# Performance work log

Hardware: AMD Instinct MI355X
Metric: run time of the kernel (lower is better)

## Reference

```python
import jax, jax.numpy as jnp
import numpy as np

DIM = 192
HEADS = 6
HEAD_DIM = 32
WS = 7          # window_size
DISP = WS // 2  # cyclic-shift displacement = 3
NEG = -1e9      # large negative instead of -inf (grad-safe, numerically equivalent)


def _rel_indices():
    idx = np.array([[x, y] for x in range(WS) for y in range(WS)])  # [WS^2, 2]
    d = idx[None, :, :] - idx[:, None, :] + WS - 1                  # [WS^2, WS^2, 2]
    return d


def _shift_masks():
    n = WS * WS
    ul = np.zeros((n, n), dtype=np.float32)
    ul[-DISP * WS:, :-DISP * WS] = NEG
    ul[:-DISP * WS, -DISP * WS:] = NEG
    lr = np.zeros((WS, WS, WS, WS), dtype=np.float32)
    lr[:, -DISP:, :, :-DISP] = NEG
    lr[:, :-DISP, :, -DISP:] = NEG
    lr = lr.reshape(n, n)
    return ul, lr


def setup_inputs() -> dict:
    key = jax.random.key(0)
    k1, k2, k3, k4, k5 = jax.random.split(key, 5)
    inner = HEADS * HEAD_DIM
    B, H, W = 32, 56, 56
    x = jax.random.normal(k1, (B, H, W, DIM), dtype=jnp.float32)
    w_qkv = jax.random.normal(k2, (DIM, inner * 3), dtype=jnp.float32) * (DIM ** -0.5)
    w_out = jax.random.normal(k3, (inner, DIM), dtype=jnp.float32) * (inner ** -0.5)
    b_out = jnp.zeros((DIM,), dtype=jnp.float32)
    pos_emb = jax.random.normal(k4, (2 * WS - 1, 2 * WS - 1), dtype=jnp.float32)
    return {"x": x, "w_qkv": w_qkv, "w_out": w_out, "b_out": b_out, "pos_emb": pos_emb}


def _forward(x, w_qkv, w_out, b_out, pos_emb):
    b, n_h, n_w, _ = x.shape
    nw_h, nw_w = n_h // WS, n_w // WS
    nw = nw_h * nw_w
    n = WS * WS
    scale = HEAD_DIM ** -0.5

    # cyclic shift
    x = jnp.roll(x, shift=(-DISP, -DISP), axis=(1, 2))

    qkv = x @ w_qkv  # [b, H, W, 3*inner]
    qkv = qkv.reshape(b, nw_h, WS, nw_w, WS, 3, HEADS, HEAD_DIM)
    # -> [3, b, heads, nw, WS*WS, head_dim]
    qkv = qkv.transpose(5, 0, 6, 1, 3, 2, 4, 7).reshape(3, b, HEADS, nw, n, HEAD_DIM)
    q, k, v = qkv[0], qkv[1], qkv[2]

    dots = jnp.einsum('bhwid,bhwjd->bhwij', q, k) * scale  # [b,h,nw,n,n]

    rel = _rel_indices()
    bias = pos_emb[rel[:, :, 0], rel[:, :, 1]]  # [n, n]
    dots = dots + bias

    # shifted-window masks: last row of windows gets UL mask, last column gets LR mask
    ul, lr = _shift_masks()
    madd = jnp.zeros((nw, n, n), dtype=dots.dtype)
    madd = madd.at[-nw_w:].add(jnp.asarray(ul))
    madd = madd.at[nw_w - 1::nw_w].add(jnp.asarray(lr))
    dots = dots + madd

    attn = jax.nn.softmax(dots, axis=-1)
    out = jnp.einsum('bhwij,bhwjd->bhwid', attn, v)  # [b,h,nw,n,hd]

    # un-window: -> [b, H, W, inner]
    out = out.reshape(b, HEADS, nw_h, nw_w, WS, WS, HEAD_DIM)
    out = out.transpose(0, 2, 4, 3, 5, 1, 6).reshape(b, n_h, n_w, HEADS * HEAD_DIM)
    out = out @ w_out + b_out

    # cyclic back-shift
    out = jnp.roll(out, shift=(DISP, DISP), axis=(1, 2))
    return out


def reference(x, w_qkv, w_out, b_out, pos_emb):
    return _forward(x, w_qkv, w_out, b_out, pos_emb)
```

## Files before the change

kernel.cpp:

```cpp
#include <hip/hip_runtime.h>
#include <hip/hip_bf16.h>


typedef __bf16 bf16x8 __attribute__((ext_vector_type(8)));
typedef __bf16 bf16x4 __attribute__((ext_vector_type(4)));
typedef float f32x4 __attribute__((ext_vector_type(4)));
using bf = __bf16;

#define MFMA16(a, b, c) __builtin_amdgcn_mfma_f32_16x16x32_bf16((a), (b), (c), 0, 0, 0)

static constexpr float kNEG = -1000000000.0f;
static constexpr float kScale = 0.17677669529663687f;

static constexpr size_t OFF_WQKVT = 0;
static constexpr size_t OFF_WOUTT = 221184;
static constexpr size_t OFF_TBL   = 294912;

static constexpr int QK_STRIDE = 40;
static constexpr int VT_STRIDE = 72;
static constexpr int X_STRIDE  = 200;
static constexpr int O_STRIDE  = 200;
static constexpr int P_STRIDE  = 72;
static constexpr int TB_STRIDE = 68;
static constexpr int R0_OFF = 0;
static constexpr int R1_OFF = 23552;
static constexpr int R2_OFF = 47104;
static constexpr int TB_OFF = 74752;
static constexpr int LDS_BYTES = TB_OFF + 49 * TB_STRIDE * 2 + 8;

__device__ __forceinline__ unsigned pack2(float a, float b) {
  union { bf h[2]; unsigned u; } cv;
  cv.h[0] = (bf)a; cv.h[1] = (bf)b;
  return cv.u;
}

__global__ void prep_kernel(const float* __restrict__ wqkv, const float* __restrict__ wout,
                            const float* __restrict__ pos, char* __restrict__ ws) {
  bf* wqkvT = (bf*)(ws + OFF_WQKVT);
  bf* woutT = (bf*)(ws + OFF_WOUTT);
  float* tbl = (float*)(ws + OFF_TBL);
  int tid = blockIdx.x * blockDim.x + threadIdx.x;
  int nthr = gridDim.x * blockDim.x;
  for (int i = tid; i < 192 * 576; i += nthr) {
    int k = i / 576, n = i % 576;
    wqkvT[n * 192 + k] = (bf)wqkv[i];
  }
  for (int i = tid; i < 192 * 192; i += nthr) {
    int k = i / 192, n = i % 192;
    woutT[n * 192 + k] = (bf)wout[i];
  }
  for (int i = tid; i < 4 * 64 * 64; i += nthr) {
    int type = i >> 12, rem = i & 4095, r = rem >> 6, c = rem & 63;
    float v;
    if (r < 49 && c < 49) {
      int ix = r / 7, iy = r % 7, jx = c / 7, jy = c % 7;
      v = pos[(jx - ix + 6) * 13 + (jy - iy + 6)];
      if ((type & 1) && ((r >= 28) != (c >= 28))) v += kNEG;
      if ((type & 2) && ((iy >= 4) != (jy >= 4))) v += kNEG;
    } else {
      v = kNEG;
    }
    tbl[i] = v;
  }
}

__global__ __launch_bounds__(512, 4) void fused_kernel(const float* __restrict__ x,
                                                       const float* __restrict__ bout,
                                                       const char* __restrict__ ws,
                                                       float* __restrict__ out) {
  __shared__ __align__(16) char smem[LDS_BYTES];
  bf* Xl = (bf*)(smem + R0_OFF);
  bf* Ql = (bf*)(smem + R0_OFF);
  bf* Pl = (bf*)(smem + R0_OFF);
  bf* Kl = (bf*)(smem + R1_OFF);
  bf* Ol = (bf*)(smem + R1_OFF);
  bf* Vl = (bf*)(smem + R2_OFF);
  bf* Tb = (bf*)(smem + TB_OFF);

  const bf* wqkvT = (const bf*)(ws + OFF_WQKVT);
  const bf* woutT = (const bf*)(ws + OFF_WOUTT);

  int bw = blockIdx.x;
  int b = bw >> 6, win = bw & 63;
  int wh = win >> 3, wwi = win & 7;
  int type = ((wh == 7) ? 1 : 0) | ((wwi == 7) ? 2 : 0);
  const float* tblg = (const float*)(ws + OFF_TBL) + type * 4096;

  int tid = threadIdx.x;
  int wave = tid >> 6, lane = tid & 63;
  int l15 = lane & 15, g = lane >> 4;
  int mrow = wave >> 2, ncol = wave & 3;

#pragma unroll
  for (int it = 0; it < 3; ++it) {
    int chunk = it * 512 + tid;
    if (chunk < 1176) {
      int r = chunk / 24, c8 = (chunk % 24) * 8;
      int tr = r / 7, tc = r % 7;
      int h = wh * 7 + tr + 3; if (h >= 56) h -= 56;
      int w = wwi * 7 + tc + 3; if (w >= 56) w -= 56;
      const float* p = x + (((size_t)b * 56 + h) * 56 + w) * 192 + c8;
      bf16x8 v;
#pragma unroll
      for (int j = 0; j < 8; ++j) v[j] = (bf)p[j];
      *(bf16x8*)(Xl + r * X_STRIDE + c8) = v;
    }
  }
  if (tid < 392) {
    int r = tid >> 3, c8 = (tid & 7) * 8;
    const float* p = tblg + r * 64 + c8;
    bf16x4 v0, v1;
#pragma unroll
    for (int j = 0; j < 4; ++j) { v0[j] = (bf)p[j]; v1[j] = (bf)p[4 + j]; }
    *(bf16x4*)(Tb + r * TB_STRIDE + c8) = v0;
    *(bf16x4*)(Tb + r * TB_STRIDE + c8 + 4) = v1;
  }
  __syncthreads();

  {
    f32x4 acc[2][6] = {};
#pragma unroll
    for (int ks = 0; ks < 6; ++ks) {
      bf16x8 a[2];
#pragma unroll
      for (int mt = 0; mt < 2; ++mt) {
        int t = mrow * 32 + mt * 16 + l15; if (t > 48) t = 48;
        a[mt] = *(const bf16x8*)(Xl + t * X_STRIDE + ks * 32 + g * 8);
      }
#pragma unroll
      for (int nt = 0; nt < 6; ++nt) {
        int n = 192 + ncol * 96 + nt * 16 + l15;
        bf16x8 bfr = *(const bf16x8*)(wqkvT + (size_t)n * 192 + ks * 32 + g * 8);
#pragma unroll
        for (int mt = 0; mt < 2; ++mt) acc[mt][nt] = MFMA16(a[mt], bfr, acc[mt][nt]);
      }
    }
#pragma unroll
    for (int nt = 0; nt < 6; ++nt) {
      int n = 192 + ncol * 96 + nt * 16 + l15;
      int s3 = n / 192;
      int lc = n - s3 * 192;
      int hd = lc >> 5, d = lc & 31;
#pragma unroll
      for (int mt = 0; mt < 2; ++mt) {
#pragma unroll
        for (int r = 0; r < 4; ++r) {
          int t = mrow * 32 + mt * 16 + 4 * g + r;
          bf bv = (bf)acc[mt][nt][r];
          if (s3 == 1) { if (t < 49) Kl[(hd * 49 + t) * QK_STRIDE + d] = bv; }
          else         { Vl[(hd * 32 + d) * VT_STRIDE + t] = bv; }
        }
      }
    }
  }

  {
    f32x4 qacc[2][3] = {};
#pragma unroll
    for (int ks = 0; ks < 6; ++ks) {
      bf16x8 a[2];
#pragma unroll
      for (int mt = 0; mt < 2; ++mt) {
        int t = mrow * 32 + mt * 16 + l15; if (t > 48) t = 48;
        a[mt] = *(const bf16x8*)(Xl + t * X_STRIDE + ks * 32 + g * 8);
      }
#pragma unroll
      for (int nt = 0; nt < 3; ++nt) {
        int n = ncol * 48 + nt * 16 + l15;
        bf16x8 bfr = *(const bf16x8*)(wqkvT + (size_t)n * 192 + ks * 32 + g * 8);
#pragma unroll
        for (int mt = 0; mt < 2; ++mt) qacc[mt][nt] = MFMA16(a[mt], bfr, qacc[mt][nt]);
      }
    }
    __syncthreads();
#pragma unroll
    for (int nt = 0; nt < 3; ++nt) {
      int n = ncol * 48 + nt * 16 + l15;
      int hd = n >> 5, d = n & 31;
#pragma unroll
      for (int mt = 0; mt < 2; ++mt) {
#pragma unroll
        for (int r = 0; r < 4; ++r) {
          int t = mrow * 32 + mt * 16 + 4 * g + r;
          if (t < 49) Ql[(hd * 49 + t) * QK_STRIDE + d] = (bf)qacc[mt][nt][r];
        }
      }
    }
  }
  __syncthreads();

  unsigned pp[3][8];
#pragma unroll
  for (int ii = 0; ii < 3; ++ii) {
    int item = wave + ii * 8;
    int head = item >> 2, mq = item & 3;
    const bf* Qh = Ql + head * 49 * QK_STRIDE;
    const bf* Kh = Kl + head * 49 * QK_STRIDE;

    int tq = mq * 16 + l15; if (tq > 48) tq = 48;
    bf16x8 qf = *(const bf16x8*)(Qh + tq * QK_STRIDE + g * 8);
    f32x4 sa[4];
#pragma unroll
    for (int nt = 0; nt < 4; ++nt) {
      int tk = nt * 16 + l15; if (tk > 48) tk = 48;
      bf16x8 kf = *(const bf16x8*)(Kh + tk * QK_STRIDE + g * 8);
      f32x4 z = {};
      sa[nt] = MFMA16(qf, kf, z);
    }
#pragma unroll
    for (int r = 0; r < 4; ++r) {
      int rowc = mq * 16 + 4 * g + r; if (rowc > 48) rowc = 48;
      const bf* trow = Tb + rowc * TB_STRIDE + l15;
#pragma unroll
      for (int nt = 0; nt < 4; ++nt)
        sa[nt][r] = sa[nt][r] * kScale + (float)trow[nt * 16];
    }

#pragma unroll
    for (int r = 0; r < 4; ++r) {
      float m = fmaxf(fmaxf(sa[0][r], sa[1][r]), fmaxf(sa[2][r], sa[3][r]));
#pragma unroll
      for (int off = 1; off < 16; off <<= 1) m = fmaxf(m, __shfl_xor(m, off));
      float p0 = __expf(sa[0][r] - m), p1 = __expf(sa[1][r] - m);
      float p2 = __expf(sa[2][r] - m), p3 = __expf(sa[3][r] - m);
      float sum = p0 + p1 + p2 + p3;
#pragma unroll
      for (int off = 1; off < 16; off <<= 1) sum += __shfl_xor(sum, off);
      float rinv = 1.0f / sum;
      pp[ii][r * 2]     = pack2(p0 * rinv, p1 * rinv);
      pp[ii][r * 2 + 1] = pack2(p2 * rinv, p3 * rinv);
    }
  }
  __syncthreads();

  bf* Pw = Pl + wave * 16 * P_STRIDE;
  for (int ii = 0; ii < 3; ++ii) {
    int item = wave + ii * 8;
    int head = item >> 2, mq = item & 3;
    const bf* Vh = Vl + head * 32 * VT_STRIDE;

#pragma unroll
    for (int r = 0; r < 4; ++r) {
      int prow = 4 * g + r;
      union { unsigned u; bf h[2]; } ua, ub;
      ua.u = pp[ii][r * 2]; ub.u = pp[ii][r * 2 + 1];
      Pw[prow * P_STRIDE + l15]      = ua.h[0];
      Pw[prow * P_STRIDE + 16 + l15] = ua.h[1];
      Pw[prow * P_STRIDE + 32 + l15] = ub.h[0];
      Pw[prow * P_STRIDE + 48 + l15] = ub.h[1];
    }
    asm volatile("s_waitcnt lgkmcnt(0)" ::: "memory");
    __builtin_amdgcn_sched_barrier(0);

    f32x4 o0 = {}, o1 = {};
#pragma unroll
    for (int ks = 0; ks < 2; ++ks) {
      bf16x8 pf = *(const bf16x8*)(Pw + l15 * P_STRIDE + ks * 32 + g * 8);
      bf16x8 v0 = *(const bf16x8*)(Vh + l15 * VT_STRIDE + ks * 32 + g * 8);
      bf16x8 v1 = *(const bf16x8*)(Vh + (16 + l15) * VT_STRIDE + ks * 32 + g * 8);
      o0 = MFMA16(pf, v0, o0);
      o1 = MFMA16(pf, v1, o1);
    }
#pragma unroll
    for (int r = 0; r < 4; ++r) {
      int orow = mq * 16 + 4 * g + r;
      if (orow < 49) {
        Ol[orow * O_STRIDE + head * 32 + l15]      = (bf)o0[r];
        Ol[orow * O_STRIDE + head * 32 + 16 + l15] = (bf)o1[r];
      }
    }
    asm volatile("s_waitcnt lgkmcnt(0)" ::: "memory");
    __builtin_amdgcn_sched_barrier(0);
  }
  __syncthreads();

  f32x4 pacc[2][3] = {};
#pragma unroll
  for (int ks = 0; ks < 6; ++ks) {
    int t0 = mrow * 32 + l15;      if (t0 > 48) t0 = 48;
    int t1 = mrow * 32 + 16 + l15; if (t1 > 48) t1 = 48;
    bf16x8 a0 = *(const bf16x8*)(Ol + t0 * O_STRIDE + ks * 32 + g * 8);
    bf16x8 a1 = *(const bf16x8*)(Ol + t1 * O_STRIDE + ks * 32 + g * 8);
#pragma unroll
    for (int nt = 0; nt < 3; ++nt) {
      bf16x8 bfr = *(const bf16x8*)(woutT + (size_t)(ncol * 48 + nt * 16 + l15) * 192 + ks * 32 + g * 8);
      pacc[0][nt] = MFMA16(a0, bfr, pacc[0][nt]);
      pacc[1][nt] = MFMA16(a1, bfr, pacc[1][nt]);
    }
  }
#pragma unroll
  for (int nt = 0; nt < 3; ++nt) {
    int col = ncol * 48 + nt * 16 + l15;
    float bo = bout[col];
#pragma unroll
    for (int mt = 0; mt < 2; ++mt) {
#pragma unroll
      for (int r = 0; r < 4; ++r) {
        int t = mrow * 32 + mt * 16 + 4 * g + r;
        if (t < 49) {
          int tr = t / 7, tc = t % 7;
          int h = wh * 7 + tr + 3; if (h >= 56) h -= 56;
          int w2 = wwi * 7 + tc + 3; if (w2 >= 56) w2 -= 56;
          out[(((size_t)b * 56 + h) * 56 + w2) * 192 + col] = pacc[mt][nt][r] + bo;
        }
      }
    }
  }
}

extern "C" void kernel_launch(void* const* d_in, const int* in_sizes, int n_in,
                              void* d_out, int out_size, void* d_ws, size_t ws_size,
                              hipStream_t stream) {
  const float* x = (const float*)d_in[0];
  const float* wqkv = (const float*)d_in[1];
  const float* wout = (const float*)d_in[2];
  const float* bout = (const float*)d_in[3];
  const float* pos = (const float*)d_in[4];
  char* ws = (char*)d_ws;

  hipLaunchKernelGGL(prep_kernel, dim3(128), dim3(256), 0, stream, wqkv, wout, pos, ws);
  hipLaunchKernelGGL(fused_kernel, dim3(2048), dim3(512), 0, stream,
                     x, bout, (const char*)ws, (float*)d_out);
}
```

Baseline: 180.0 us.

## Compute transposed QK^T so softmax probabilities feed PV MFMA from registers

```diff
diff --git a/kernel.cpp b/kernel.cpp
--- a/kernel.cpp
+++ b/kernel.cpp
@@ -20,7 +20,6 @@
 static constexpr int VT_STRIDE = 72;
 static constexpr int X_STRIDE  = 200;
 static constexpr int O_STRIDE  = 200;
-static constexpr int P_STRIDE  = 72;
 static constexpr int TB_STRIDE = 68;
 static constexpr int R0_OFF = 0;
 static constexpr int R1_OFF = 23552;
@@ -71,7 +70,6 @@
   __shared__ __align__(16) char smem[LDS_BYTES];
   bf* Xl = (bf*)(smem + R0_OFF);
   bf* Ql = (bf*)(smem + R0_OFF);
-  bf* Pl = (bf*)(smem + R0_OFF);
   bf* Kl = (bf*)(smem + R1_OFF);
   bf* Ol = (bf*)(smem + R1_OFF);
   bf* Vl = (bf*)(smem + R2_OFF);
@@ -189,7 +187,7 @@
   }
   __syncthreads();
 
-  unsigned pp[3][8];
+  unsigned pp[3][4][2];
 #pragma unroll
   for (int ii = 0; ii < 3; ++ii) {
     int item = wave + ii * 8;
@@ -197,69 +195,61 @@
     const bf* Qh = Ql + head * 49 * QK_STRIDE;
     const bf* Kh = Kl + head * 49 * QK_STRIDE;
 
-    int tq = mq * 16 + l15; if (tq > 48) tq = 48;
-    bf16x8 qf = *(const bf16x8*)(Qh + tq * QK_STRIDE + g * 8);
+    int q = mq * 16 + l15;
+    int qc = q > 48 ? 48 : q;
+    bf16x8 qf = *(const bf16x8*)(Qh + qc * QK_STRIDE + g * 8);
+
     f32x4 sa[4];
 #pragma unroll
-    for (int nt = 0; nt < 4; ++nt) {
-      int tk = nt * 16 + l15; if (tk > 48) tk = 48;
-      bf16x8 kf = *(const bf16x8*)(Kh + tk * QK_STRIDE + g * 8);
+    for (int T = 0; T < 4; ++T) {
+      int kt = ((l15 >> 2) << 3) + ((T & 1) << 2) + ((T >> 1) << 5) + (l15 & 3);
+      int ktc = kt > 48 ? 48 : kt;
+      bf16x8 kf = *(const bf16x8*)(Kh + ktc * QK_STRIDE + g * 8);
       f32x4 z = {};
-      sa[nt] = MFMA16(qf, kf, z);
-    }
-#pragma unroll
-    for (int r = 0; r < 4; ++r) {
-      int rowc = mq * 16 + 4 * g + r; if (rowc > 48) rowc = 48;
-      const bf* trow = Tb + rowc * TB_STRIDE + l15;
-#pragma unroll
-      for (int nt = 0; nt < 4; ++nt)
-        sa[nt][r] = sa[nt][r] * kScale + (float)trow[nt * 16];
-    }
-
-#pragma unroll
-    for (int r = 0; r < 4; ++r) {
-      float m = fmaxf(fmaxf(sa[0][r], sa[1][r]), fmaxf(sa[2][r], sa[3][r]));
-#pragma unroll
-      for (int off = 1; off < 16; off <<= 1) m = fmaxf(m, __shfl_xor(m, off));
-      float p0 = __expf(sa[0][r] - m), p1 = __expf(sa[1][r] - m);
-      float p2 = __expf(sa[2][r] - m), p3 = __expf(sa[3][r] - m);
-      float sum = p0 + p1 + p2 + p3;
-#pragma unroll
-      for (int off = 1; off < 16; off <<= 1) sum += __shfl_xor(sum, off);
-      float rinv = 1.0f / sum;
-      pp[ii][r * 2]     = pack2(p0 * rinv, p1 * rinv);
-      pp[ii][r * 2 + 1] = pack2(p2 * rinv, p3 * rinv);
+      sa[T] = MFMA16(kf, qf, z);
+    }
+
+    float e[4][4];
+    float lsum = 0.0f;
+#pragma unroll
+    for (int T = 0; T < 4; ++T) {
+      int cb = (g << 3) + ((T & 1) << 2) + ((T >> 1) << 5);
+      bf16x4 bias = *(const bf16x4*)(Tb + qc * TB_STRIDE + cb);
+#pragma unroll
+      for (int r = 0; r < 4; ++r) {
+        float ev = __expf(sa[T][r] * kScale + (float)bias[r]);
+        e[T][r] = ev;
+        lsum += ev;
+      }
+    }
+    lsum += __shfl_xor(lsum, 16);
+    lsum += __shfl_xor(lsum, 32);
+    float rinv = 1.0f / lsum;
+#pragma unroll
+    for (int T = 0; T < 4; ++T) {
+      pp[ii][T][0] = pack2(e[T][0] * rinv, e[T][1] * rinv);
+      pp[ii][T][1] = pack2(e[T][2] * rinv, e[T][3] * rinv);
     }
   }
   __syncthreads();
 
-  bf* Pw = Pl + wave * 16 * P_STRIDE;
   for (int ii = 0; ii < 3; ++ii) {
     int item = wave + ii * 8;
     int head = item >> 2, mq = item & 3;
     const bf* Vh = Vl + head * 32 * VT_STRIDE;
 
-#pragma unroll
-    for (int r = 0; r < 4; ++r) {
-      int prow = 4 * g + r;
-      union { unsigned u; bf h[2]; } ua, ub;
-      ua.u = pp[ii][r * 2]; ub.u = pp[ii][r * 2 + 1];
-      Pw[prow * P_STRIDE + l15]      = ua.h[0];
-      Pw[prow * P_STRIDE + 16 + l15] = ua.h[1];
-      Pw[prow * P_STRIDE + 32 + l15] = ub.h[0];
-      Pw[prow * P_STRIDE + 48 + l15] = ub.h[1];
-    }
-    asm volatile("s_waitcnt lgkmcnt(0)" ::: "memory");
-    __builtin_amdgcn_sched_barrier(0);
-
     f32x4 o0 = {}, o1 = {};
 #pragma unroll
     for (int ks = 0; ks < 2; ++ks) {
-      bf16x8 pf = *(const bf16x8*)(Pw + l15 * P_STRIDE + ks * 32 + g * 8);
+      union { unsigned u[4]; bf16x8 v; } af;
+      af.u[0] = pp[ii][2 * ks][0];
+      af.u[1] = pp[ii][2 * ks][1];
+      af.u[2] = pp[ii][2 * ks + 1][0];
+      af.u[3] = pp[ii][2 * ks + 1][1];
       bf16x8 v0 = *(const bf16x8*)(Vh + l15 * VT_STRIDE + ks * 32 + g * 8);
       bf16x8 v1 = *(const bf16x8*)(Vh + (16 + l15) * VT_STRIDE + ks * 32 + g * 8);
-      o0 = MFMA16(pf, v0, o0);
-      o1 = MFMA16(pf, v1, o1);
+      o0 = MFMA16(af.v, v0, o0);
+      o1 = MFMA16(af.v, v1, o1);
     }
 #pragma unroll
     for (int r = 0; r < 4; ++r) {
@@ -269,8 +259,6 @@
         Ol[orow * O_STRIDE + head * 32 + 16 + l15] = (bf)o1[r];
       }
     }
-    asm volatile("s_waitcnt lgkmcnt(0)" ::: "memory");
-    __builtin_amdgcn_sched_barrier(0);
   }
   __syncthreads();
 
```

Result: faster. 172.9 us (-4.0%).
